# Performance work log

Hardware: AMD Instinct MI355X
Metric: run time of the kernel (lower is better)

Reference implementation:

```python
import jax, jax.numpy as jnp
import numpy as np

B, S, D, H = 2, 2048, 1024, 16
DK = D // H


def setup_inputs() -> dict:
    key = jax.random.key(0)
    ks = jax.random.split(key, 11)
    def lin(k):
        kw, kb = jax.random.split(k)
        bound = 1.0 / np.sqrt(D)
        w = jax.random.uniform(kw, (D, D), jnp.float32, -bound, bound)
        b = jax.random.uniform(kb, (D,), jnp.float32, -bound, bound)
        return w, b
    wq_w, wq_b = lin(ks[0])
    wk_w, wk_b = lin(ks[1])
    wv_w, wv_b = lin(ks[2])
    wo_w, wo_b = lin(ks[3])
    q = jax.random.normal(ks[4], (B, S, D), jnp.float32)
    k = jax.random.normal(ks[5], (B, S, D), jnp.float32)
    v = jax.random.normal(ks[6], (B, S, D), jnp.float32)
    # causal mask, broadcastable to (B, H, S, S); 0 -> masked
    mask = jnp.tril(jnp.ones((S, S), jnp.int32))[None, None, :, :]
    return {"q": q, "k": k, "v": v, "mask": mask,
            "wq_w": wq_w, "wq_b": wq_b, "wk_w": wk_w, "wk_b": wk_b,
            "wv_w": wv_w, "wv_b": wv_b, "wo_w": wo_w, "wo_b": wo_b}


def reference(q, k, v, mask, wq_w, wq_b, wk_w, wk_b, wv_w, wv_b, wo_w, wo_b):
    # projections (torch Linear: x @ W^T + b)
    def split_heads(x):  # (B,S,D) -> (B,H,S,DK)
        return x.reshape(B, S, H, DK).transpose(0, 2, 1, 3)
    Q = split_heads(q @ wq_w.T + wq_b)
    K = split_heads(k @ wk_w.T + wk_b)
    V = split_heads(v @ wv_w.T + wv_b)
    scores = jnp.einsum('bhqd,bhkd->bhqk', Q, K) / np.sqrt(DK).astype(np.float32)
    scores = jnp.where(mask == 0, jnp.float32(-1e9), scores)
    attn = jax.nn.softmax(scores, axis=-1)
    out = jnp.einsum('bhqk,bhkd->bhqd', attn, V)  # (B,H,S,DK)
    out = out.transpose(0, 2, 1, 3).reshape(B, S, D)
    return out @ wo_w.T + wo_b
```

## Files before the change

kernel.cpp:

```cpp
#include <hip/hip_runtime.h>

#define DEV __device__ __forceinline__

typedef __attribute__((ext_vector_type(8))) short short8;
typedef __attribute__((ext_vector_type(4))) float f32x4;
typedef __bf16 bf16x8 __attribute__((ext_vector_type(8)));
typedef unsigned int u32;
typedef unsigned short u16;

constexpr int Bb = 2, Ss = 2048, Dd = 1024, Hh = 16, DKc = 64;
constexpr int Kk = 1024;

#define QSCALE 0.1803368801111204f

DEV u16 f2bf(float f) {
  u32 u = __builtin_bit_cast(u32, f);
  u32 r = (u + 0x7fffu + ((u >> 16) & 1u)) >> 16;
  return (u16)r;
}

DEV u32 pk_bf16(float lo, float hi) {
  u32 w;
  asm("v_cvt_pk_bf16_f32 %0, %1, %2" : "=v"(w) : "v"(lo), "v"(hi));
  return w;
}

DEV f32x4 mfma16(short8 a, short8 b, f32x4 c) {
  return __builtin_amdgcn_mfma_f32_16x16x32_bf16(
      __builtin_bit_cast(bf16x8, a), __builtin_bit_cast(bf16x8, b), c, 0, 0, 0);
}

DEV void gload_lds16(const u16* g, u16* lds) {
  __builtin_amdgcn_global_load_lds(
      (const __attribute__((address_space(1))) u32*)g,
      (__attribute__((address_space(3))) u32*)lds, 16, 0, 0);
}

struct CvtArgs {
  const float* in[7];
  u16* out[7];
  int n[7];
};

__global__ __launch_bounds__(256) void cvt_all(CvtArgs a) {
  int z = blockIdx.z;
  int i = (blockIdx.x * 256 + threadIdx.x) * 4;
  if (i >= a.n[z]) return;
  float4 v = *reinterpret_cast<const float4*>(a.in[z] + i);
  ushort4 o;
  o.x = f2bf(v.x); o.y = f2bf(v.y); o.z = f2bf(v.z); o.w = f2bf(v.w);
  *reinterpret_cast<ushort4*>(a.out[z] + i) = o;
}

template<int MT, int NT>
DEV void gemm_core(const u16* __restrict__ A, const u16* __restrict__ Bt,
                   u16* smA, u16* smB, f32x4 (&acc)[MT][NT], int gm0, int gn0) {
  constexpr int NSTEP = Kk / 32;
  constexpr int SA = MT * 1024;
  constexpr int SB = NT * 1024;
  constexpr int S = MT / 2 + NT / 2;
  const int tid = threadIdx.x;
  const int w = tid >> 6, l = tid & 63;
  const int g = (l >> 4) & 3, r = l & 15;
  const int wm = w >> 1, wn = w & 1;
  const int srow = l >> 2, scol = (l & 3) * 8;

  auto stage = [&](int buf, int kt) {
    int kb = kt * 32;
#pragma unroll
    for (int cc = 0; cc < MT / 2; ++cc) {
      int c = w + cc * 4;
      gload_lds16(A + (size_t)(gm0 + c * 16 + srow) * Kk + kb + scol,
                  smA + buf * SA + c * 512);
    }
#pragma unroll
    for (int cc = 0; cc < NT / 2; ++cc) {
      int c = w + cc * 4;
      gload_lds16(Bt + (size_t)(gn0 + c * 16 + srow) * Kk + kb + scol,
                  smB + buf * SB + c * 512);
    }
  };

  stage(0, 0);
  stage(1, 1);
  for (int kt = 0; kt < NSTEP; ++kt) {
    const int buf = kt % 3;
    if (kt + 1 < NSTEP) {
      if constexpr (S == 4) asm volatile("s_waitcnt vmcnt(4)" ::: "memory");
      else                  asm volatile("s_waitcnt vmcnt(3)" ::: "memory");
    } else {
      asm volatile("s_waitcnt vmcnt(0)" ::: "memory");
    }
    __builtin_amdgcn_s_barrier();
    __builtin_amdgcn_sched_barrier(0);
    if (kt + 2 < NSTEP) stage((kt + 2) % 3, kt + 2);

    short8 af[MT], bf_[NT];
#pragma unroll
    for (int t = 0; t < MT; ++t)
      af[t] = *reinterpret_cast<const short8*>(
          smA + buf * SA + (wm * (MT * 16) + t * 16 + r) * 32 + g * 8);
#pragma unroll
    for (int t = 0; t < NT; ++t)
      bf_[t] = *reinterpret_cast<const short8*>(
          smB + buf * SB + (wn * (NT * 16) + t * 16 + r) * 32 + g * 8);
    __builtin_amdgcn_s_setprio(1);
#pragma unroll
    for (int mt = 0; mt < MT; ++mt)
#pragma unroll
      for (int nt = 0; nt < NT; ++nt)
        acc[mt][nt] = mfma16(af[mt], bf_[nt], acc[mt][nt]);
    __builtin_amdgcn_s_setprio(0);
  }
}

__global__ __launch_bounds__(256, 3) void proj_qkv(
    const u16* __restrict__ xq, const u16* __restrict__ xk, const u16* __restrict__ xv,
    const u16* __restrict__ Wq, const u16* __restrict__ Wk, const u16* __restrict__ Wv,
    const float* __restrict__ bq, const float* __restrict__ bk, const float* __restrict__ bv,
    u16* __restrict__ Qh, u16* __restrict__ Kh, u16* __restrict__ Vt) {
  __shared__ u16 smA[3 * 128 * 32], smB[3 * 128 * 32];
  const int flat = (blockIdx.z * 32 + blockIdx.y) * 8 + blockIdx.x;
  const int nid = (flat & 7) * 96 + (flat >> 3);
  const int bx = nid & 7, by = (nid >> 3) & 31, z = nid >> 8;
  const u16* A = z == 0 ? xq : (z == 1 ? xk : xv);
  const u16* W = z == 0 ? Wq : (z == 1 ? Wk : Wv);
  const float* bias = z == 0 ? bq : (z == 1 ? bk : bv);
  u16* out = z == 0 ? Qh : (z == 1 ? Kh : Vt);
  const float sc = z == 0 ? QSCALE : 1.0f;
  const int gm0 = by * 128, gn0 = bx * 128;
  f32x4 acc[4][4] = {};
  gemm_core<4, 4>(A, W, smA, smB, acc, gm0, gn0);

  const int tid = threadIdx.x;
  const int w = tid >> 6, l = tid & 63, g = (l >> 4) & 3, r = l & 15;
  const int wm = w >> 1, wn = w & 1;
#pragma unroll
  for (int mt = 0; mt < 4; ++mt) {
#pragma unroll
    for (int nt = 0; nt < 4; ++nt) {
      int ncol = gn0 + wn * 64 + nt * 16 + r;
      int h = ncol >> 6, dk = ncol & 63;
      float bb = bias[ncol];
      int mrow0 = gm0 + wm * 64 + mt * 16 + g * 4;
      int b = mrow0 >> 11, s0 = mrow0 & 2047;
      if (z < 2) {
#pragma unroll
        for (int i = 0; i < 4; ++i)
          out[(((size_t)b * Hh + h) * Ss + s0 + i) * DKc + dk] =
              f2bf((acc[mt][nt][i] + bb) * sc);
      } else {
        ushort4 ov;
        ov.x = f2bf(acc[mt][nt][0] + bb);
        ov.y = f2bf(acc[mt][nt][1] + bb);
        ov.z = f2bf(acc[mt][nt][2] + bb);
        ov.w = f2bf(acc[mt][nt][3] + bb);
        *reinterpret_cast<ushort4*>(
            &out[(((size_t)b * Hh + h) * DKc + dk) * Ss + s0]) = ov;
      }
    }
  }
}

__global__ __launch_bounds__(256, 2) void attn(
    const u16* __restrict__ Qh, const u16* __restrict__ Kh,
    const u16* __restrict__ Vt, u16* __restrict__ Ob) {
  __shared__ u16 smK[4][64 * 64];
  __shared__ u16 smV[4][64 * 64];
  __shared__ u16 smP[4][16 * 72];

  const int fid = blockIdx.y * 16 + blockIdx.x;
  const int xcd = fid & 7, slot = fid >> 3;
  const int bh = xcd * 4 + (slot >> 4);
  const int pair = slot & 15;
  const int bidx = bh >> 4, h = bh & 15;

  const int tid = threadIdx.x, w = tid >> 6, l = tid & 63;
  const int g = (l >> 4) & 3, r = l & 15;

  const u16* Qb = Qh + (size_t)bh * Ss * DKc;
  const u16* Kb = Kh + (size_t)bh * Ss * DKc;
  const u16* Vb = Vt + (size_t)bh * DKc * Ss;
  u16* Pw = smP[w];

  const int srow0 = tid >> 3, schunk = tid & 7;

  auto stage = [&](int sl, int kb) {
#pragma unroll
    for (int j = 0; j < 2; ++j) {
      int row = j * 32 + srow0;
      int c = schunk ^ (row & 7);
      u16* dK = smK[sl] + (j * 256 + w * 64) * 8;
      u16* dV = smV[sl] + (j * 256 + w * 64) * 8;
      gload_lds16(Kb + (size_t)(kb + row) * DKc + c * 8, dK);
      gload_lds16(Vb + (size_t)row * Ss + kb + c * 8, dV);
    }
  };

  for (int t2 = 0; t2 < 2; ++t2) {
    const int qt = (t2 == 0) ? (31 - pair) : pair;
    const int ntile = qt + 1;
    const int npair = (ntile + 1) >> 1;
    const int qw = qt * 64 + w * 16;
    const int q = qw + r;

    if (t2) __builtin_amdgcn_s_barrier();

    short8 qf[2];
    qf[0] = *reinterpret_cast<const short8*>(Qb + (size_t)q * DKc + g * 8);
    qf[1] = *reinterpret_cast<const short8*>(Qb + (size_t)q * DKc + 32 + g * 8);

    stage(0, 0);
    if (ntile > 1) stage(1, 64);

    f32x4 o[4] = {};
    float m_s = -3e38f, l_s = 0.f;

    for (int pp = 0; pp < npair; ++pp) {
      const int slotA = (pp & 1) * 2;
      const int kbA = pp * 128;
      const bool hasB = (2 * pp + 1 < ntile);
      const bool diagA = (2 * pp == qt);
      const bool diagB = hasB && (2 * pp + 1 == qt);

      asm volatile("s_waitcnt vmcnt(0)" ::: "memory");
      __builtin_amdgcn_s_barrier();
      __builtin_amdgcn_sched_barrier(0);
      if (pp + 1 < npair) {
        int nb = ((pp + 1) & 1) * 2;
        stage(nb, kbA + 128);
        if (2 * pp + 3 < ntile) stage(nb + 1, kbA + 192);
      }

      f32x4 sA[4] = {}, sB[4] = {};
      __builtin_amdgcn_s_setprio(1);
#pragma unroll
      for (int ks = 0; ks < 2; ++ks)
#pragma unroll
        for (int nt = 0; nt < 4; ++nt) {
          int row = nt * 16 + r;
          int ch = (ks * 4 + g) ^ (row & 7);
          short8 kf = *reinterpret_cast<const short8*>(&smK[slotA][row * 64 + ch * 8]);
          sA[nt] = mfma16(kf, qf[ks], sA[nt]);
        }
      if (hasB) {
#pragma unroll
        for (int ks = 0; ks < 2; ++ks)
#pragma unroll
          for (int nt = 0; nt < 4; ++nt) {
            int row = nt * 16 + r;
            int ch = (ks * 4 + g) ^ (row & 7);
            short8 kf = *reinterpret_cast<const short8*>(&smK[slotA + 1][row * 64 + ch * 8]);
            sB[nt] = mfma16(kf, qf[ks], sB[nt]);
          }
      }
      __builtin_amdgcn_s_setprio(0);

      const int qloc = w * 16 + r;
      if (diagA) {
#pragma unroll
        for (int nt = 0; nt < 4; ++nt)
#pragma unroll
          for (int i = 0; i < 4; ++i)
            if (nt * 16 + g * 4 + i > qloc) sA[nt][i] = -1e30f;
      }
      if (diagB) {
#pragma unroll
        for (int nt = 0; nt < 4; ++nt)
#pragma unroll
          for (int i = 0; i < 4; ++i)
            if (nt * 16 + g * 4 + i > qloc) sB[nt][i] = -1e30f;
      }

      float mx0 = fmaxf(fmaxf(sA[0][0], sA[0][1]), fmaxf(sA[0][2], sA[0][3]));
      float mx1 = fmaxf(fmaxf(sA[1][0], sA[1][1]), fmaxf(sA[1][2], sA[1][3]));
      float mx2 = fmaxf(fmaxf(sA[2][0], sA[2][1]), fmaxf(sA[2][2], sA[2][3]));
      float mx3 = fmaxf(fmaxf(sA[3][0], sA[3][1]), fmaxf(sA[3][2], sA[3][3]));
      float mx = fmaxf(fmaxf(mx0, mx1), fmaxf(mx2, mx3));
      if (hasB) {
        float nx0 = fmaxf(fmaxf(sB[0][0], sB[0][1]), fmaxf(sB[0][2], sB[0][3]));
        float nx1 = fmaxf(fmaxf(sB[1][0], sB[1][1]), fmaxf(sB[1][2], sB[1][3]));
        float nx2 = fmaxf(fmaxf(sB[2][0], sB[2][1]), fmaxf(sB[2][2], sB[2][3]));
        float nx3 = fmaxf(fmaxf(sB[3][0], sB[3][1]), fmaxf(sB[3][2], sB[3][3]));
        mx = fmaxf(mx, fmaxf(fmaxf(nx0, nx1), fmaxf(nx2, nx3)));
      }

      if (__any(mx > m_s + 8.f)) {
        float mr = fmaxf(mx, __shfl_xor(mx, 16));
        mr = fmaxf(mr, __shfl_xor(mr, 32));
        float mn = fmaxf(m_s, mr);
        float f = __builtin_amdgcn_exp2f(m_s - mn);
        m_s = mn;
        l_s *= f;
#pragma unroll
        for (int dt = 0; dt < 4; ++dt) {
          o[dt][0] *= f; o[dt][1] *= f; o[dt][2] *= f; o[dt][3] *= f;
        }
      }

#pragma unroll
      for (int nt = 0; nt < 4; ++nt) {
        float p0 = __builtin_amdgcn_exp2f(sA[nt][0] - m_s);
        float p1 = __builtin_amdgcn_exp2f(sA[nt][1] - m_s);
        float p2 = __builtin_amdgcn_exp2f(sA[nt][2] - m_s);
        float p3 = __builtin_amdgcn_exp2f(sA[nt][3] - m_s);
        l_s += (p0 + p1) + (p2 + p3);
        *reinterpret_cast<u32*>(&Pw[r * 72 + nt * 16 + g * 4])     = pk_bf16(p0, p1);
        *reinterpret_cast<u32*>(&Pw[r * 72 + nt * 16 + g * 4 + 2]) = pk_bf16(p2, p3);
      }
      __builtin_amdgcn_s_setprio(1);
#pragma unroll
      for (int ks = 0; ks < 2; ++ks) {
        short8 pf = *reinterpret_cast<const short8*>(&Pw[r * 72 + ks * 32 + g * 8]);
#pragma unroll
        for (int dt = 0; dt < 4; ++dt) {
          int row = dt * 16 + r;
          int ch = (ks * 4 + g) ^ (row & 7);
          short8 vf = *reinterpret_cast<const short8*>(&smV[slotA][row * 64 + ch * 8]);
          o[dt] = mfma16(vf, pf, o[dt]);
        }
      }
      __builtin_amdgcn_s_setprio(0);

      if (hasB) {
#pragma unroll
        for (int nt = 0; nt < 4; ++nt) {
          float p0 = __builtin_amdgcn_exp2f(sB[nt][0] - m_s);
          float p1 = __builtin_amdgcn_exp2f(sB[nt][1] - m_s);
          float p2 = __builtin_amdgcn_exp2f(sB[nt][2] - m_s);
          float p3 = __builtin_amdgcn_exp2f(sB[nt][3] - m_s);
          l_s += (p0 + p1) + (p2 + p3);
          *reinterpret_cast<u32*>(&Pw[r * 72 + nt * 16 + g * 4])     = pk_bf16(p0, p1);
          *reinterpret_cast<u32*>(&Pw[r * 72 + nt * 16 + g * 4 + 2]) = pk_bf16(p2, p3);
        }
        __builtin_amdgcn_s_setprio(1);
#pragma unroll
        for (int ks = 0; ks < 2; ++ks) {
          short8 pf = *reinterpret_cast<const short8*>(&Pw[r * 72 + ks * 32 + g * 8]);
#pragma unroll
          for (int dt = 0; dt < 4; ++dt) {
            int row = dt * 16 + r;
            int ch = (ks * 4 + g) ^ (row & 7);
            short8 vf = *reinterpret_cast<const short8*>(&smV[slotA + 1][row * 64 + ch * 8]);
            o[dt] = mfma16(vf, pf, o[dt]);
          }
        }
        __builtin_amdgcn_s_setprio(0);
      }
    }

    float lt = l_s;
    lt += __shfl_xor(lt, 16);
    lt += __shfl_xor(lt, 32);
    float inv = 1.f / lt;
    size_t ro = ((size_t)bidx * Ss + q) * Dd + h * DKc;
#pragma unroll
    for (int dt = 0; dt < 4; ++dt) {
      ushort4 ov;
      ov.x = f2bf(o[dt][0] * inv);
      ov.y = f2bf(o[dt][1] * inv);
      ov.z = f2bf(o[dt][2] * inv);
      ov.w = f2bf(o[dt][3] * inv);
      *reinterpret_cast<ushort4*>(&Ob[ro + dt * 16 + g * 4]) = ov;
    }
  }
}

__global__ __launch_bounds__(256, 2) void gemm_out(
    const u16* __restrict__ Ob, const u16* __restrict__ Wo,
    const float* __restrict__ bo, float* __restrict__ out) {
  __shared__ u16 smA[3 * 64 * 32], smB[3 * 128 * 32];
  const int flat = blockIdx.y * 8 + blockIdx.x;
  const int nid = (flat & 7) * 64 + (flat >> 3);
  const int bx = nid & 7, by = nid >> 3;
  const int gm0 = by * 64, gn0 = bx * 128;
  f32x4 acc[2][4] = {};
  gemm_core<2, 4>(Ob, Wo, smA, smB, acc, gm0, gn0);

  const int tid = threadIdx.x;
  const int w = tid >> 6, l = tid & 63, g = (l >> 4) & 3, r = l & 15;
  const int wm = w >> 1, wn = w & 1;
#pragma unroll
  for (int mt = 0; mt < 2; ++mt) {
#pragma unroll
    for (int nt = 0; nt < 4; ++nt) {
      int ncol = gn0 + wn * 64 + nt * 16 + r;
      float bb = bo[ncol];
#pragma unroll
      for (int i = 0; i < 4; ++i) {
        int mrow = gm0 + wm * 32 + mt * 16 + g * 4 + i;
        out[(size_t)mrow * Dd + ncol] = acc[mt][nt][i] + bb;
      }
    }
  }
}

extern "C" void kernel_launch(void* const* d_in, const int* in_sizes, int n_in,
                              void* d_out, int out_size, void* d_ws, size_t ws_size,
                              hipStream_t stream) {
  const float* q    = (const float*)d_in[0];
  const float* k    = (const float*)d_in[1];
  const float* v    = (const float*)d_in[2];
  const float* wq_w = (const float*)d_in[4];
  const float* wq_b = (const float*)d_in[5];
  const float* wk_w = (const float*)d_in[6];
  const float* wk_b = (const float*)d_in[7];
  const float* wv_w = (const float*)d_in[8];
  const float* wv_b = (const float*)d_in[9];
  const float* wo_w = (const float*)d_in[10];
  const float* wo_b = (const float*)d_in[11];

  char* ws = (char*)d_ws;
  u16* xq  = (u16*)(ws + 0);
  u16* xk  = (u16*)(ws + 8388608);
  u16* xv  = (u16*)(ws + 16777216);
  u16* Wqb = (u16*)(ws + 25165824);
  u16* Wkb = (u16*)(ws + 27262976);
  u16* Wvb = (u16*)(ws + 29360128);
  u16* Wob = (u16*)(ws + 31457280);
  u16* Qh  = (u16*)(ws + 33554432);
  u16* Kh  = (u16*)(ws + 41943040);
  u16* Vt  = (u16*)(ws + 50331648);
  u16* Ob  = (u16*)(ws + 0);

  CvtArgs ca;
  ca.in[0] = q;    ca.out[0] = xq;  ca.n[0] = 4194304;
  ca.in[1] = k;    ca.out[1] = xk;  ca.n[1] = 4194304;
  ca.in[2] = v;    ca.out[2] = xv;  ca.n[2] = 4194304;
  ca.in[3] = wq_w; ca.out[3] = Wqb; ca.n[3] = 1048576;
  ca.in[4] = wk_w; ca.out[4] = Wkb; ca.n[4] = 1048576;
  ca.in[5] = wv_w; ca.out[5] = Wvb; ca.n[5] = 1048576;
  ca.in[6] = wo_w; ca.out[6] = Wob; ca.n[6] = 1048576;

  cvt_all<<<dim3(4096, 1, 7), 256, 0, stream>>>(ca);
  proj_qkv<<<dim3(8, 32, 3), 256, 0, stream>>>(xq, xk, xv, Wqb, Wkb, Wvb,
                                               wq_b, wk_b, wv_b, Qh, Kh, Vt);
  attn<<<dim3(16, 32), 256, 0, stream>>>(Qh, Kh, Vt, Ob);
  gemm_out<<<dim3(8, 64), 256, 0, stream>>>(Ob, Wob, wo_b, (float*)d_out);
}
```

Baseline: 112.7 us.

## Load V fragments directly from global, one q-tile per block, raise occupancy

V tiles are no longer staged into shared memory. Each wave now reads its V MFMA fragments straight from global memory into registers, which halves the LDS footprint and allows launch bounds of 3 blocks per CU. The grid changes from 512 blocks that each handled a paired long and short query tile to 1024 blocks that each handle one query tile, ordered longest first. The risks are uncoalesced strided global reads of V that are exposed to latency, more registers for the V fragments, and weaker load balancing than the paired scheme.

```diff
diff --git a/kernel.cpp b/kernel.cpp
--- a/kernel.cpp
+++ b/kernel.cpp
@@ -162,17 +162,16 @@
   }
 }
 
-__global__ __launch_bounds__(256, 2) void attn(
+__global__ __launch_bounds__(256, 3) void attn(
     const u16* __restrict__ Qh, const u16* __restrict__ Kh,
     const u16* __restrict__ Vt, u16* __restrict__ Ob) {
   __shared__ u16 smK[4][64 * 64];
-  __shared__ u16 smV[4][64 * 64];
   __shared__ u16 smP[4][16 * 72];
 
-  const int fid = blockIdx.y * 16 + blockIdx.x;
+  const int fid = blockIdx.y * 8 + blockIdx.x;
   const int xcd = fid & 7, slot = fid >> 3;
-  const int bh = xcd * 4 + (slot >> 4);
-  const int pair = slot & 15;
+  const int bh = xcd * 4 + (slot >> 5);
+  const int qt = 31 - (slot & 31);
   const int bidx = bh >> 4, h = bh & 15;
 
   const int tid = threadIdx.x, w = tid >> 6, l = tid & 63;
@@ -190,49 +189,71 @@
     for (int j = 0; j < 2; ++j) {
       int row = j * 32 + srow0;
       int c = schunk ^ (row & 7);
-      u16* dK = smK[sl] + (j * 256 + w * 64) * 8;
-      u16* dV = smV[sl] + (j * 256 + w * 64) * 8;
-      gload_lds16(Kb + (size_t)(kb + row) * DKc + c * 8, dK);
-      gload_lds16(Vb + (size_t)row * Ss + kb + c * 8, dV);
+      gload_lds16(Kb + (size_t)(kb + row) * DKc + c * 8,
+                  smK[sl] + (j * 256 + w * 64) * 8);
     }
   };
 
-  for (int t2 = 0; t2 < 2; ++t2) {
-    const int qt = (t2 == 0) ? (31 - pair) : pair;
-    const int ntile = qt + 1;
-    const int npair = (ntile + 1) >> 1;
-    const int qw = qt * 64 + w * 16;
-    const int q = qw + r;
-
-    if (t2) __builtin_amdgcn_s_barrier();
-
-    short8 qf[2];
-    qf[0] = *reinterpret_cast<const short8*>(Qb + (size_t)q * DKc + g * 8);
-    qf[1] = *reinterpret_cast<const short8*>(Qb + (size_t)q * DKc + 32 + g * 8);
-
-    stage(0, 0);
-    if (ntile > 1) stage(1, 64);
-
-    f32x4 o[4] = {};
-    float m_s = -3e38f, l_s = 0.f;
-
-    for (int pp = 0; pp < npair; ++pp) {
-      const int slotA = (pp & 1) * 2;
-      const int kbA = pp * 128;
-      const bool hasB = (2 * pp + 1 < ntile);
-      const bool diagA = (2 * pp == qt);
-      const bool diagB = hasB && (2 * pp + 1 == qt);
-
-      asm volatile("s_waitcnt vmcnt(0)" ::: "memory");
-      __builtin_amdgcn_s_barrier();
-      __builtin_amdgcn_sched_barrier(0);
-      if (pp + 1 < npair) {
-        int nb = ((pp + 1) & 1) * 2;
-        stage(nb, kbA + 128);
-        if (2 * pp + 3 < ntile) stage(nb + 1, kbA + 192);
-      }
-
-      f32x4 sA[4] = {}, sB[4] = {};
+  const int ntile = qt + 1;
+  const int npair = (ntile + 1) >> 1;
+  const int qw = qt * 64 + w * 16;
+  const int q = qw + r;
+
+  short8 qf[2];
+  qf[0] = *reinterpret_cast<const short8*>(Qb + (size_t)q * DKc + g * 8);
+  qf[1] = *reinterpret_cast<const short8*>(Qb + (size_t)q * DKc + 32 + g * 8);
+
+  stage(0, 0);
+  if (ntile > 1) stage(1, 64);
+
+  f32x4 o[4] = {};
+  float m_s = -3e38f, l_s = 0.f;
+
+  for (int pp = 0; pp < npair; ++pp) {
+    const int slotA = (pp & 1) * 2;
+    const int kbA = pp * 128;
+    const bool hasB = (2 * pp + 1 < ntile);
+    const bool diagA = (2 * pp == qt);
+    const bool diagB = hasB && (2 * pp + 1 == qt);
+
+    asm volatile("s_waitcnt vmcnt(0)" ::: "memory");
+    __builtin_amdgcn_s_barrier();
+    __builtin_amdgcn_sched_barrier(0);
+    if (pp + 1 < npair) {
+      int nb = ((pp + 1) & 1) * 2;
+      stage(nb, kbA + 128);
+      if (2 * pp + 3 < ntile) stage(nb + 1, kbA + 192);
+    }
+
+    short8 vA[8];
+#pragma unroll
+    for (int ks = 0; ks < 2; ++ks)
+#pragma unroll
+      for (int dt = 0; dt < 4; ++dt)
+        vA[ks * 4 + dt] = *reinterpret_cast<const short8*>(
+            Vb + (size_t)(dt * 16 + r) * Ss + kbA + ks * 32 + g * 8);
+
+    f32x4 sA[4] = {}, sB[4] = {};
+    __builtin_amdgcn_s_setprio(1);
+#pragma unroll
+    for (int ks = 0; ks < 2; ++ks)
+#pragma unroll
+      for (int nt = 0; nt < 4; ++nt) {
+        int row = nt * 16 + r;
+        int ch = (ks * 4 + g) ^ (row & 7);
+        short8 kf = *reinterpret_cast<const short8*>(&smK[slotA][row * 64 + ch * 8]);
+        sA[nt] = mfma16(kf, qf[ks], sA[nt]);
+      }
+    __builtin_amdgcn_s_setprio(0);
+
+    short8 vB[8];
+    if (hasB) {
+#pragma unroll
+      for (int ks = 0; ks < 2; ++ks)
+#pragma unroll
+        for (int dt = 0; dt < 4; ++dt)
+          vB[ks * 4 + dt] = *reinterpret_cast<const short8*>(
+              Vb + (size_t)(dt * 16 + r) * Ss + kbA + 64 + ks * 32 + g * 8);
       __builtin_amdgcn_s_setprio(1);
 #pragma unroll
       for (int ks = 0; ks < 2; ++ks)
@@ -240,70 +261,81 @@
         for (int nt = 0; nt < 4; ++nt) {
           int row = nt * 16 + r;
           int ch = (ks * 4 + g) ^ (row & 7);
-          short8 kf = *reinterpret_cast<const short8*>(&smK[slotA][row * 64 + ch * 8]);
-          sA[nt] = mfma16(kf, qf[ks], sA[nt]);
+          short8 kf = *reinterpret_cast<const short8*>(&smK[slotA + 1][row * 64 + ch * 8]);
+          sB[nt] = mfma16(kf, qf[ks], sB[nt]);
         }
-      if (hasB) {
-#pragma unroll
-        for (int ks = 0; ks < 2; ++ks)
-#pragma unroll
-          for (int nt = 0; nt < 4; ++nt) {
-            int row = nt * 16 + r;
-            int ch = (ks * 4 + g) ^ (row & 7);
-            short8 kf = *reinterpret_cast<const short8*>(&smK[slotA + 1][row * 64 + ch * 8]);
-            sB[nt] = mfma16(kf, qf[ks], sB[nt]);
-          }
-      }
       __builtin_amdgcn_s_setprio(0);
-
-      const int qloc = w * 16 + r;
-      if (diagA) {
-#pragma unroll
-        for (int nt = 0; nt < 4; ++nt)
-#pragma unroll
-          for (int i = 0; i < 4; ++i)
-            if (nt * 16 + g * 4 + i > qloc) sA[nt][i] = -1e30f;
-      }
-      if (diagB) {
-#pragma unroll
-        for (int nt = 0; nt < 4; ++nt)
-#pragma unroll
-          for (int i = 0; i < 4; ++i)
-            if (nt * 16 + g * 4 + i > qloc) sB[nt][i] = -1e30f;
-      }
-
-      float mx0 = fmaxf(fmaxf(sA[0][0], sA[0][1]), fmaxf(sA[0][2], sA[0][3]));
-      float mx1 = fmaxf(fmaxf(sA[1][0], sA[1][1]), fmaxf(sA[1][2], sA[1][3]));
-      float mx2 = fmaxf(fmaxf(sA[2][0], sA[2][1]), fmaxf(sA[2][2], sA[2][3]));
-      float mx3 = fmaxf(fmaxf(sA[3][0], sA[3][1]), fmaxf(sA[3][2], sA[3][3]));
-      float mx = fmaxf(fmaxf(mx0, mx1), fmaxf(mx2, mx3));
-      if (hasB) {
-        float nx0 = fmaxf(fmaxf(sB[0][0], sB[0][1]), fmaxf(sB[0][2], sB[0][3]));
-        float nx1 = fmaxf(fmaxf(sB[1][0], sB[1][1]), fmaxf(sB[1][2], sB[1][3]));
-        float nx2 = fmaxf(fmaxf(sB[2][0], sB[2][1]), fmaxf(sB[2][2], sB[2][3]));
-        float nx3 = fmaxf(fmaxf(sB[3][0], sB[3][1]), fmaxf(sB[3][2], sB[3][3]));
-        mx = fmaxf(mx, fmaxf(fmaxf(nx0, nx1), fmaxf(nx2, nx3)));
-      }
-
-      if (__any(mx > m_s + 8.f)) {
-        float mr = fmaxf(mx, __shfl_xor(mx, 16));
-        mr = fmaxf(mr, __shfl_xor(mr, 32));
-        float mn = fmaxf(m_s, mr);
-        float f = __builtin_amdgcn_exp2f(m_s - mn);
-        m_s = mn;
-        l_s *= f;
-#pragma unroll
-        for (int dt = 0; dt < 4; ++dt) {
-          o[dt][0] *= f; o[dt][1] *= f; o[dt][2] *= f; o[dt][3] *= f;
-        }
-      }
-
+    }
+
+    const int qloc = w * 16 + r;
+    if (diagA) {
+#pragma unroll
+      for (int nt = 0; nt < 4; ++nt)
+#pragma unroll
+        for (int i = 0; i < 4; ++i)
+          if (nt * 16 + g * 4 + i > qloc) sA[nt][i] = -1e30f;
+    }
+    if (diagB) {
+#pragma unroll
+      for (int nt = 0; nt < 4; ++nt)
+#pragma unroll
+        for (int i = 0; i < 4; ++i)
+          if (nt * 16 + g * 4 + i > qloc) sB[nt][i] = -1e30f;
+    }
+
+    float mx0 = fmaxf(fmaxf(sA[0][0], sA[0][1]), fmaxf(sA[0][2], sA[0][3]));
+    float mx1 = fmaxf(fmaxf(sA[1][0], sA[1][1]), fmaxf(sA[1][2], sA[1][3]));
+    float mx2 = fmaxf(fmaxf(sA[2][0], sA[2][1]), fmaxf(sA[2][2], sA[2][3]));
+    float mx3 = fmaxf(fmaxf(sA[3][0], sA[3][1]), fmaxf(sA[3][2], sA[3][3]));
+    float mx = fmaxf(fmaxf(mx0, mx1), fmaxf(mx2, mx3));
+    if (hasB) {
+      float nx0 = fmaxf(fmaxf(sB[0][0], sB[0][1]), fmaxf(sB[0][2], sB[0][3]));
+      float nx1 = fmaxf(fmaxf(sB[1][0], sB[1][1]), fmaxf(sB[1][2], sB[1][3]));
+      float nx2 = fmaxf(fmaxf(sB[2][0], sB[2][1]), fmaxf(sB[2][2], sB[2][3]));
+      float nx3 = fmaxf(fmaxf(sB[3][0], sB[3][1]), fmaxf(sB[3][2], sB[3][3]));
+      mx = fmaxf(mx, fmaxf(fmaxf(nx0, nx1), fmaxf(nx2, nx3)));
+    }
+
+    if (__any(mx > m_s + 8.f)) {
+      float mr = fmaxf(mx, __shfl_xor(mx, 16));
+      mr = fmaxf(mr, __shfl_xor(mr, 32));
+      float mn = fmaxf(m_s, mr);
+      float f = __builtin_amdgcn_exp2f(m_s - mn);
+      m_s = mn;
+      l_s *= f;
+#pragma unroll
+      for (int dt = 0; dt < 4; ++dt) {
+        o[dt][0] *= f; o[dt][1] *= f; o[dt][2] *= f; o[dt][3] *= f;
+      }
+    }
+
+#pragma unroll
+    for (int nt = 0; nt < 4; ++nt) {
+      float p0 = __builtin_amdgcn_exp2f(sA[nt][0] - m_s);
+      float p1 = __builtin_amdgcn_exp2f(sA[nt][1] - m_s);
+      float p2 = __builtin_amdgcn_exp2f(sA[nt][2] - m_s);
+      float p3 = __builtin_amdgcn_exp2f(sA[nt][3] - m_s);
+      l_s += (p0 + p1) + (p2 + p3);
+      *reinterpret_cast<u32*>(&Pw[r * 72 + nt * 16 + g * 4])     = pk_bf16(p0, p1);
+      *reinterpret_cast<u32*>(&Pw[r * 72 + nt * 16 + g * 4 + 2]) = pk_bf16(p2, p3);
+    }
+    __builtin_amdgcn_s_setprio(1);
+#pragma unroll
+    for (int ks = 0; ks < 2; ++ks) {
+      short8 pf = *reinterpret_cast<const short8*>(&Pw[r * 72 + ks * 32 + g * 8]);
+#pragma unroll
+      for (int dt = 0; dt < 4; ++dt)
+        o[dt] = mfma16(vA[ks * 4 + dt], pf, o[dt]);
+    }
+    __builtin_amdgcn_s_setprio(0);
+
+    if (hasB) {
 #pragma unroll
       for (int nt = 0; nt < 4; ++nt) {
-        float p0 = __builtin_amdgcn_exp2f(sA[nt][0] - m_s);
-        float p1 = __builtin_amdgcn_exp2f(sA[nt][1] - m_s);
-        float p2 = __builtin_amdgcn_exp2f(sA[nt][2] - m_s);
-        float p3 = __builtin_amdgcn_exp2f(sA[nt][3] - m_s);
+        float p0 = __builtin_amdgcn_exp2f(sB[nt][0] - m_s);
+        float p1 = __builtin_amdgcn_exp2f(sB[nt][1] - m_s);
+        float p2 = __builtin_amdgcn_exp2f(sB[nt][2] - m_s);
+        float p3 = __builtin_amdgcn_exp2f(sB[nt][3] - m_s);
         l_s += (p0 + p1) + (p2 + p3);
         *reinterpret_cast<u32*>(&Pw[r * 72 + nt * 16 + g * 4])     = pk_bf16(p0, p1);
         *reinterpret_cast<u32*>(&Pw[r * 72 + nt * 16 + g * 4 + 2]) = pk_bf16(p2, p3);
@@ -313,56 +345,26 @@
       for (int ks = 0; ks < 2; ++ks) {
         short8 pf = *reinterpret_cast<const short8*>(&Pw[r * 72 + ks * 32 + g * 8]);
 #pragma unroll
-        for (int dt = 0; dt < 4; ++dt) {
-          int row = dt * 16 + r;
-          int ch = (ks * 4 + g) ^ (row & 7);
-          short8 vf = *reinterpret_cast<const short8*>(&smV[slotA][row * 64 + ch * 8]);
-          o[dt] = mfma16(vf, pf, o[dt]);
-        }
+        for (int dt = 0; dt < 4; ++dt)
+          o[dt] = mfma16(vB[ks * 4 + dt], pf, o[dt]);
       }
       __builtin_amdgcn_s_setprio(0);
-
-      if (hasB) {
-#pragma unroll
-        for (int nt = 0; nt < 4; ++nt) {
-          float p0 = __builtin_amdgcn_exp2f(sB[nt][0] - m_s);
-          float p1 = __builtin_amdgcn_exp2f(sB[nt][1] - m_s);
-          float p2 = __builtin_amdgcn_exp2f(sB[nt][2] - m_s);
-          float p3 = __builtin_amdgcn_exp2f(sB[nt][3] - m_s);
-          l_s += (p0 + p1) + (p2 + p3);
-          *reinterpret_cast<u32*>(&Pw[r * 72 + nt * 16 + g * 4])     = pk_bf16(p0, p1);
-          *reinterpret_cast<u32*>(&Pw[r * 72 + nt * 16 + g * 4 + 2]) = pk_bf16(p2, p3);
-        }
-        __builtin_amdgcn_s_setprio(1);
-#pragma unroll
-        for (int ks = 0; ks < 2; ++ks) {
-          short8 pf = *reinterpret_cast<const short8*>(&Pw[r * 72 + ks * 32 + g * 8]);
-#pragma unroll
-          for (int dt = 0; dt < 4; ++dt) {
-            int row = dt * 16 + r;
-            int ch = (ks * 4 + g) ^ (row & 7);
-            short8 vf = *reinterpret_cast<const short8*>(&smV[slotA + 1][row * 64 + ch * 8]);
-            o[dt] = mfma16(vf, pf, o[dt]);
-          }
-        }
-        __builtin_amdgcn_s_setprio(0);
-      }
-    }
-
-    float lt = l_s;
-    lt += __shfl_xor(lt, 16);
-    lt += __shfl_xor(lt, 32);
-    float inv = 1.f / lt;
-    size_t ro = ((size_t)bidx * Ss + q) * Dd + h * DKc;
-#pragma unroll
-    for (int dt = 0; dt < 4; ++dt) {
-      ushort4 ov;
-      ov.x = f2bf(o[dt][0] * inv);
-      ov.y = f2bf(o[dt][1] * inv);
-      ov.z = f2bf(o[dt][2] * inv);
-      ov.w = f2bf(o[dt][3] * inv);
-      *reinterpret_cast<ushort4*>(&Ob[ro + dt * 16 + g * 4]) = ov;
-    }
+    }
+  }
+
+  float lt = l_s;
+  lt += __shfl_xor(lt, 16);
+  lt += __shfl_xor(lt, 32);
+  float inv = 1.f / lt;
+  size_t ro = ((size_t)bidx * Ss + q) * Dd + h * DKc;
+#pragma unroll
+  for (int dt = 0; dt < 4; ++dt) {
+    ushort4 ov;
+    ov.x = f2bf(o[dt][0] * inv);
+    ov.y = f2bf(o[dt][1] * inv);
+    ov.z = f2bf(o[dt][2] * inv);
+    ov.w = f2bf(o[dt][3] * inv);
+    *reinterpret_cast<ushort4*>(&Ob[ro + dt * 16 + g * 4]) = ov;
   }
 }
 
@@ -435,6 +437,6 @@
   cvt_all<<<dim3(4096, 1, 7), 256, 0, stream>>>(ca);
   proj_qkv<<<dim3(8, 32, 3), 256, 0, stream>>>(xq, xk, xv, Wqb, Wkb, Wvb,
                                                wq_b, wk_b, wv_b, Qh, Kh, Vt);
-  attn<<<dim3(16, 32), 256, 0, stream>>>(Qh, Kh, Vt, Ob);
+  attn<<<dim3(8, 128), 256, 0, stream>>>(Qh, Kh, Vt, Ob);
   gemm_out<<<dim3(8, 64), 256, 0, stream>>>(Ob, Wob, wo_b, (float*)d_out);
 }
```

Result: slower. 169.0 us (+50.0%).

## Fuse fp32-to-bf16 activation conversion into QKV projection GEMM loads

Applied to the files above, without the earlier changes.

The QKV projection now reads fp32 activations directly, converting them to bf16 in registers before writing to LDS, with a register double-buffered prefetch pipeline and its own vmcnt waits. The separate conversion pass over q/k/v is dropped, so the cvt kernel only handles the weights. This removes a full write and re-read of the bf16 activation copies, at the cost of more global traffic and register pressure inside the GEMM. Block-to-tile swizzles in both GEMMs are also remapped to change L2 locality.

```diff
diff --git a/kernel.cpp b/kernel.cpp
--- a/kernel.cpp
+++ b/kernel.cpp
@@ -4,6 +4,7 @@
 
 typedef __attribute__((ext_vector_type(8))) short short8;
 typedef __attribute__((ext_vector_type(4))) float f32x4;
+typedef __attribute__((ext_vector_type(4))) unsigned int u32x4;
 typedef __bf16 bf16x8 __attribute__((ext_vector_type(8)));
 typedef unsigned int u32;
 typedef unsigned short u16;
@@ -37,9 +38,9 @@
 }
 
 struct CvtArgs {
-  const float* in[7];
-  u16* out[7];
-  int n[7];
+  const float* in[4];
+  u16* out[4];
+  int n[4];
 };
 
 __global__ __launch_bounds__(256) void cvt_all(CvtArgs a) {
@@ -114,23 +115,102 @@
   }
 }
 
+template<int MT, int NT>
+DEV void gemm_core_mix(const float* __restrict__ A, const u16* __restrict__ Bt,
+                       u16* smA, u16* smB, f32x4 (&acc)[MT][NT], int gm0, int gn0) {
+  constexpr int NSTEP = Kk / 32;
+  constexpr int SA = MT * 1024, SB = NT * 1024;
+  const int tid = threadIdx.x;
+  const int w = tid >> 6, l = tid & 63;
+  const int g = (l >> 4) & 3, r = l & 15;
+  const int wm = w >> 1, wn = w & 1;
+  const int srow = l >> 2, scol = (l & 3) * 8;
+
+  float4 a0[MT / 2][2], a1[MT / 2][2];
+
+  auto loadA = [&](float4 (&dst)[MT / 2][2], int kt) {
+    int kb = kt * 32;
+#pragma unroll
+    for (int c = 0; c < MT / 2; ++c) {
+      int p = tid + c * 256;
+      const float* src = A + (size_t)(gm0 + (p >> 2)) * Kk + kb + (p & 3) * 8;
+      dst[c][0] = *reinterpret_cast<const float4*>(src);
+      dst[c][1] = *reinterpret_cast<const float4*>(src + 4);
+    }
+  };
+  auto writeA = [&](float4 (&s)[MT / 2][2], int buf) {
+#pragma unroll
+    for (int c = 0; c < MT / 2; ++c) {
+      int p = tid + c * 256;
+      u32x4 wv;
+      wv.x = pk_bf16(s[c][0].x, s[c][0].y);
+      wv.y = pk_bf16(s[c][0].z, s[c][0].w);
+      wv.z = pk_bf16(s[c][1].x, s[c][1].y);
+      wv.w = pk_bf16(s[c][1].z, s[c][1].w);
+      *reinterpret_cast<u32x4*>(smA + buf * SA + p * 8) = wv;
+    }
+  };
+  auto stageB = [&](int buf, int kt) {
+    int kb = kt * 32;
+#pragma unroll
+    for (int cc = 0; cc < NT / 2; ++cc) {
+      int c = w + cc * 4;
+      gload_lds16(Bt + (size_t)(gn0 + c * 16 + srow) * Kk + kb + scol,
+                  smB + buf * SB + c * 512);
+    }
+  };
+
+  loadA(a0, 0); stageB(0, 0);
+  loadA(a1, 1); stageB(1, 1);
+  for (int kt = 0; kt < NSTEP; ++kt) {
+    const int bufA = kt & 1, bufB = kt % 3;
+    if (kt & 1) { writeA(a1, bufA); if (kt + 2 < NSTEP) loadA(a1, kt + 2); }
+    else        { writeA(a0, bufA); if (kt + 2 < NSTEP) loadA(a0, kt + 2); }
+    if (kt + 2 < NSTEP)      asm volatile("s_waitcnt vmcnt(10)" ::: "memory");
+    else if (kt + 1 < NSTEP) asm volatile("s_waitcnt vmcnt(6)" ::: "memory");
+    else                     asm volatile("s_waitcnt vmcnt(0)" ::: "memory");
+    asm volatile("s_waitcnt lgkmcnt(0)" ::: "memory");
+    __builtin_amdgcn_s_barrier();
+    __builtin_amdgcn_sched_barrier(0);
+    if (kt + 2 < NSTEP) stageB((kt + 2) % 3, kt + 2);
+
+    short8 af[MT], bf_[NT];
+#pragma unroll
+    for (int t = 0; t < MT; ++t)
+      af[t] = *reinterpret_cast<const short8*>(
+          smA + bufA * SA + (wm * (MT * 16) + t * 16 + r) * 32 + g * 8);
+#pragma unroll
+    for (int t = 0; t < NT; ++t)
+      bf_[t] = *reinterpret_cast<const short8*>(
+          smB + bufB * SB + (wn * (NT * 16) + t * 16 + r) * 32 + g * 8);
+    __builtin_amdgcn_s_setprio(1);
+#pragma unroll
+    for (int mt = 0; mt < MT; ++mt)
+#pragma unroll
+      for (int nt = 0; nt < NT; ++nt)
+        acc[mt][nt] = mfma16(af[mt], bf_[nt], acc[mt][nt]);
+    __builtin_amdgcn_s_setprio(0);
+  }
+}
+
 __global__ __launch_bounds__(256, 3) void proj_qkv(
-    const u16* __restrict__ xq, const u16* __restrict__ xk, const u16* __restrict__ xv,
+    const float* __restrict__ xq, const float* __restrict__ xk, const float* __restrict__ xv,
     const u16* __restrict__ Wq, const u16* __restrict__ Wk, const u16* __restrict__ Wv,
     const float* __restrict__ bq, const float* __restrict__ bk, const float* __restrict__ bv,
     u16* __restrict__ Qh, u16* __restrict__ Kh, u16* __restrict__ Vt) {
-  __shared__ u16 smA[3 * 128 * 32], smB[3 * 128 * 32];
+  __shared__ u16 smA[2 * 4096], smB[3 * 4096];
   const int flat = (blockIdx.z * 32 + blockIdx.y) * 8 + blockIdx.x;
-  const int nid = (flat & 7) * 96 + (flat >> 3);
-  const int bx = nid & 7, by = (nid >> 3) & 31, z = nid >> 8;
-  const u16* A = z == 0 ? xq : (z == 1 ? xk : xv);
+  const int zby = (flat & 7) * 12 + ((flat >> 3) % 12);
+  const int bx = flat / 96;
+  const int z = zby >> 5, by = zby & 31;
+  const float* A = z == 0 ? xq : (z == 1 ? xk : xv);
   const u16* W = z == 0 ? Wq : (z == 1 ? Wk : Wv);
   const float* bias = z == 0 ? bq : (z == 1 ? bk : bv);
   u16* out = z == 0 ? Qh : (z == 1 ? Kh : Vt);
   const float sc = z == 0 ? QSCALE : 1.0f;
   const int gm0 = by * 128, gn0 = bx * 128;
   f32x4 acc[4][4] = {};
-  gemm_core<4, 4>(A, W, smA, smB, acc, gm0, gn0);
+  gemm_core_mix<4, 4>(A, W, smA, smB, acc, gm0, gn0);
 
   const int tid = threadIdx.x;
   const int w = tid >> 6, l = tid & 63, g = (l >> 4) & 3, r = l & 15;
@@ -371,8 +451,8 @@
     const float* __restrict__ bo, float* __restrict__ out) {
   __shared__ u16 smA[3 * 64 * 32], smB[3 * 128 * 32];
   const int flat = blockIdx.y * 8 + blockIdx.x;
-  const int nid = (flat & 7) * 64 + (flat >> 3);
-  const int bx = nid & 7, by = nid >> 3;
+  const int by = (flat & 7) * 8 + ((flat >> 3) & 7);
+  const int bx = flat >> 6;
   const int gm0 = by * 64, gn0 = bx * 128;
   f32x4 acc[2][4] = {};
   gemm_core<2, 4>(Ob, Wo, smA, smB, acc, gm0, gn0);
@@ -411,9 +491,6 @@
   const float* wo_b = (const float*)d_in[11];
 
   char* ws = (char*)d_ws;
-  u16* xq  = (u16*)(ws + 0);
-  u16* xk  = (u16*)(ws + 8388608);
-  u16* xv  = (u16*)(ws + 16777216);
   u16* Wqb = (u16*)(ws + 25165824);
   u16* Wkb = (u16*)(ws + 27262976);
   u16* Wvb = (u16*)(ws + 29360128);
@@ -424,16 +501,13 @@
   u16* Ob  = (u16*)(ws + 0);
 
   CvtArgs ca;
-  ca.in[0] = q;    ca.out[0] = xq;  ca.n[0] = 4194304;
-  ca.in[1] = k;    ca.out[1] = xk;  ca.n[1] = 4194304;
-  ca.in[2] = v;    ca.out[2] = xv;  ca.n[2] = 4194304;
-  ca.in[3] = wq_w; ca.out[3] = Wqb; ca.n[3] = 1048576;
-  ca.in[4] = wk_w; ca.out[4] = Wkb; ca.n[4] = 1048576;
-  ca.in[5] = wv_w; ca.out[5] = Wvb; ca.n[5] = 1048576;
-  ca.in[6] = wo_w; ca.out[6] = Wob; ca.n[6] = 1048576;
-
-  cvt_all<<<dim3(4096, 1, 7), 256, 0, stream>>>(ca);
-  proj_qkv<<<dim3(8, 32, 3), 256, 0, stream>>>(xq, xk, xv, Wqb, Wkb, Wvb,
+  ca.in[0] = wq_w; ca.out[0] = Wqb; ca.n[0] = 1048576;
+  ca.in[1] = wk_w; ca.out[1] = Wkb; ca.n[1] = 1048576;
+  ca.in[2] = wv_w; ca.out[2] = Wvb; ca.n[2] = 1048576;
+  ca.in[3] = wo_w; ca.out[3] = Wob; ca.n[3] = 1048576;
+
+  cvt_all<<<dim3(1024, 1, 4), 256, 0, stream>>>(ca);
+  proj_qkv<<<dim3(8, 32, 3), 256, 0, stream>>>(q, k, v, Wqb, Wkb, Wvb,
                                                wq_b, wk_b, wv_b, Qh, Kh, Vt);
   attn<<<dim3(16, 32), 256, 0, stream>>>(Qh, Kh, Vt, Ob);
   gemm_out<<<dim3(8, 64), 256, 0, stream>>>(Ob, Wob, wo_b, (float*)d_out);
```

After: 109.5 us (median of 2 runs). 1.03x faster.
